# Kernel tuning notes

Measured on AMD Instinct MI355X. Metric: run time of the kernel, lower is better.

## Reference

```python
import jax, jax.numpy as jnp
import numpy as np

LN_EPS = 1e-5


def setup_inputs() -> dict:
    key = jax.random.key(0)
    ks = jax.random.split(key, 4)
    B, N, E, H = 2, 512, 128, 256
    h = jax.random.normal(ks[0], (B, N, E), dtype=jnp.float32)
    gamma = jnp.ones((E,), dtype=jnp.float32)
    beta = jnp.zeros((E,), dtype=jnp.float32)
    # First Linear: in_dim = 2E, out_dim = H. Stored as [2E, H] (x @ W1 + b1).
    W1 = jax.random.normal(ks[1], (2 * E, H), dtype=jnp.float32) / np.sqrt(2 * E)
    b1 = jnp.zeros((H,), dtype=jnp.float32)
    # Second Linear: [H, 1] squeezed to [H], scalar bias.
    w2 = jax.random.normal(ks[2], (H,), dtype=jnp.float32) / np.sqrt(H)
    b2 = jnp.zeros((), dtype=jnp.float32)
    return {"h": h, "gamma": gamma, "beta": beta, "W1": W1, "b1": b1,
            "w2": w2, "b2": b2}


def reference(h, gamma, beta, W1, b1, w2, b2):
    # LayerNorm over E
    mu = jnp.mean(h, axis=-1, keepdims=True)
    var = jnp.mean(jnp.square(h - mu), axis=-1, keepdims=True)
    h_n = (h - mu) * jax.lax.rsqrt(var + LN_EPS) * gamma + beta  # [B,N,E]

    E = h_n.shape[-1]
    # Decompose Linear(concat(h_i, h_j)) = h_i @ Wa + h_j @ Wb + b1
    Wa, Wb = W1[:E], W1[E:]
    a = jnp.einsum('bne,eh->bnh', h_n, Wa)  # contribution of first slot
    b = jnp.einsum('bne,eh->bnh', h_n, Wb)  # contribution of second slot
    # Pairwise pre-activation for the (i,j) ordering: [B,N,N,H]
    z_ij = a[:, :, None, :] + b[:, None, :, :] + b1
    g = jax.nn.gelu(z_ij, approximate=False)  # torch GELU is exact (erf)
    l_ij = jnp.einsum('bijh,h->bij', g, w2) + b2  # [B,N,N]
    # l_ji[b,i,j] == l_ij[b,j,i], so reuse via transpose (same math as
    # running the MLP twice on swapped concat order).
    return 0.5 * (l_ij + jnp.swapaxes(l_ij, 1, 2))
```

## Files before the change

### kernel.cpp

```cpp
#include <hip/hip_runtime.h>
#include <math.h>

#define EDIM 128
#define HDIM 256
#define NDIM 512
#define BDIM 2
#define LN_EPS 1e-5f

typedef float v2f __attribute__((ext_vector_type(2)));

__global__ __launch_bounds__(256) void k_ln_proj(
    const float* __restrict__ hptr, const float* __restrict__ gamma,
    const float* __restrict__ beta, const float* __restrict__ W1,
    const float* __restrict__ b1, float* __restrict__ a_out,
    float* __restrict__ b_out)
{
    __shared__ float hn_s[4][EDIM];
    const int tid = threadIdx.x;
    const int r = tid >> 6;
    const int lane = tid & 63;
    const int row0 = blockIdx.x * 4;
    const float2 v = *(const float2*)(hptr + (row0 + r) * EDIM + lane * 2);
    float s  = v.x + v.y;
    float ss = v.x * v.x + v.y * v.y;
    #pragma unroll
    for (int k = 32; k >= 1; k >>= 1) {
        s  += __shfl_xor(s, k, 64);
        ss += __shfl_xor(ss, k, 64);
    }
    const float mu  = s * (1.0f / EDIM);
    const float var = ss * (1.0f / EDIM) - mu * mu;
    const float rs  = rsqrtf(var + LN_EPS);
    const float2 g2 = *(const float2*)(gamma + lane * 2);
    const float2 be = *(const float2*)(beta + lane * 2);
    hn_s[r][lane * 2]     = (v.x - mu) * rs * g2.x + be.x;
    hn_s[r][lane * 2 + 1] = (v.y - mu) * rs * g2.y + be.y;
    __syncthreads();
    float sa0 = 0.f, sa1 = 0.f, sa2 = 0.f, sa3 = 0.f;
    float sb0 = 0.f, sb1 = 0.f, sb2 = 0.f, sb3 = 0.f;
    #pragma unroll 4
    for (int e = 0; e < EDIM; ++e) {
        const float wa = W1[e * HDIM + tid];
        const float wb = W1[(EDIM + e) * HDIM + tid];
        const float h0 = hn_s[0][e], h1 = hn_s[1][e];
        const float h2 = hn_s[2][e], h3 = hn_s[3][e];
        sa0 = fmaf(h0, wa, sa0); sa1 = fmaf(h1, wa, sa1);
        sa2 = fmaf(h2, wa, sa2); sa3 = fmaf(h3, wa, sa3);
        sb0 = fmaf(h0, wb, sb0); sb1 = fmaf(h1, wb, sb1);
        sb2 = fmaf(h2, wb, sb2); sb3 = fmaf(h3, wb, sb3);
    }
    const float bb1 = b1[tid];
    a_out[(row0 + 0) * HDIM + tid] = sa0;
    a_out[(row0 + 1) * HDIM + tid] = sa1;
    a_out[(row0 + 2) * HDIM + tid] = sa2;
    a_out[(row0 + 3) * HDIM + tid] = sa3;
    b_out[(row0 + 0) * HDIM + tid] = sb0 + bb1;
    b_out[(row0 + 1) * HDIM + tid] = sb1 + bb1;
    b_out[(row0 + 2) * HDIM + tid] = sb2 + bb1;
    b_out[(row0 + 3) * HDIM + tid] = sb3 + bb1;
}

__device__ __forceinline__ v2f gelu2(v2f z) {
    const v2f c2 = {-0.10294826f, -0.10294826f};
    const v2f c1 = {-2.3022082f, -2.3022082f};
    const v2f z2 = z * z;
    const v2f q  = __builtin_elementwise_fma(c2, z2, c1);
    const v2f p  = z * q;
    v2f e;
    e.x = __builtin_amdgcn_exp2f(p.x);
    e.y = __builtin_amdgcn_exp2f(p.y);
    const v2f d = e + 1.0f;
    v2f r;
    r.x = __builtin_amdgcn_rcpf(d.x);
    r.y = __builtin_amdgcn_rcpf(d.y);
    return z * r;
}

#define HHALF 128
#define PAD 132

__global__ __launch_bounds__(256, 6) void k_pair(
    const float* __restrict__ a, const float* __restrict__ bpb,
    const float* __restrict__ w2, float* __restrict__ pout)
{
    __shared__ float a_s[32][PAD];
    __shared__ float b_s[16][PAD];
    __shared__ float w2_s[HHALF];
    const int blk = blockIdx.x;
    const int hh = blk & 1;
    const int bj = (blk >> 1) & 31;
    const int bi = (blk >> 6) & 15;
    const int bb = blk >> 10;
    const int tid = threadIdx.x;
    const int hho = hh * HHALF;

    const float* arow = a + (bb * NDIM + bi * 32) * HDIM + hho;
    const float* brow = bpb + (bb * NDIM + bj * 16) * HDIM + hho;

    if (tid < HHALF / 4) ((float4*)w2_s)[tid] = ((const float4*)(w2 + hho))[tid];

    #pragma unroll
    for (int idx = tid; idx < 1536; idx += 256) {
        if (idx < 1024) {
            const int r = idx >> 5, c = idx & 31;
        *(float4*)&a_s[r][c * 4] = *(const float4*)(arow + r * HDIM + c * 4);
        } else {
            const int k = idx - 1024;
            const int r = k >> 5, c = k & 31;
            *(float4*)&b_s[r][c * 4] = *(const float4*)(brow + r * HDIM + c * 4);
        }
    }
    __syncthreads();

    const int ti = tid >> 4, tj = tid & 15;
    const float* ap0 = a_s[ti];
    const float* ap1 = a_s[ti + 16];
    const float* bp  = b_s[tj];
    v2f acc0 = {0.f, 0.f}, acc1 = {0.f, 0.f};

    #pragma unroll 4
    for (int h4 = 0; h4 < HHALF; h4 += 4) {
        const float4 a0 = *(const float4*)(ap0 + h4);
        const float4 a1 = *(const float4*)(ap1 + h4);
        const float4 b0 = *(const float4*)(bp + h4);
        const float4 wv = *(const float4*)(w2_s + h4);
        const v2f alo0 = {a0.x, a0.y}, ahi0 = {a0.z, a0.w};
        const v2f alo1 = {a1.x, a1.y}, ahi1 = {a1.z, a1.w};
        const v2f blo  = {b0.x, b0.y}, bhi  = {b0.z, b0.w};
        const v2f wlo  = {wv.x, wv.y}, whi  = {wv.z, wv.w};
        acc0 = __builtin_elementwise_fma(wlo, gelu2(alo0 + blo), acc0);
        acc0 = __builtin_elementwise_fma(whi, gelu2(ahi0 + bhi), acc0);
        acc1 = __builtin_elementwise_fma(wlo, gelu2(alo1 + blo), acc1);
        acc1 = __builtin_elementwise_fma(whi, gelu2(ahi1 + bhi), acc1);
    }
    const int i0 = bi * 32 + ti;
    const int j0 = bj * 16 + tj;
    float* ob = pout + (size_t)hh * (BDIM * NDIM * NDIM) + (bb * NDIM + i0) * NDIM + j0;
    ob[0]         = acc0.x + acc0.y;
    ob[16 * NDIM] = acc1.x + acc1.y;
}

__global__ __launch_bounds__(256) void k_sym(const float* __restrict__ p,
                                             float* __restrict__ out,
                                             const float* __restrict__ b2) {
    __shared__ float Ta[32][33];
    __shared__ float Tb[32][33];
    const int blk = blockIdx.x;
    const int b  = blk >> 8;
    const int ti = (blk >> 4) & 15;
    const int tj = blk & 15;
    if (tj < ti) return;
    const float bias = b2[0];
    const float* p0 = p + (size_t)b * NDIM * NDIM;
    const float* p1 = p0 + (size_t)BDIM * NDIM * NDIM;
    float* base = out + (size_t)b * NDIM * NDIM;
    const int tx = threadIdx.x & 31;
    const int ty = threadIdx.x >> 5;
    #pragma unroll
    for (int r = ty; r < 32; r += 8) {
        const int ia = (ti * 32 + r) * NDIM + tj * 32 + tx;
        const int ib = (tj * 32 + r) * NDIM + ti * 32 + tx;
        Ta[r][tx] = p0[ia] + p1[ia];
        Tb[r][tx] = p0[ib] + p1[ib];
    }
    __syncthreads();
    #pragma unroll
    for (int r = ty; r < 32; r += 8) {
        base[(ti * 32 + r) * NDIM + tj * 32 + tx] = 0.5f * (Ta[r][tx] + Tb[tx][r]) + bias;
    }
    if (ti != tj) {
        #pragma unroll
        for (int r = ty; r < 32; r += 8) {
            base[(tj * 32 + r) * NDIM + ti * 32 + tx] = 0.5f * (Tb[r][tx] + Ta[tx][r]) + bias;
        }
    }
}

extern "C" void kernel_launch(void* const* d_in, const int* in_sizes, int n_in,
                              void* d_out, int out_size, void* d_ws, size_t ws_size,
                              hipStream_t stream) {
    const float* hptr  = (const float*)d_in[0];
    const float* gamma = (const float*)d_in[1];
    const float* beta  = (const float*)d_in[2];
    const float* W1    = (const float*)d_in[3];
    const float* b1    = (const float*)d_in[4];
    const float* w2    = (const float*)d_in[5];
    const float* b2    = (const float*)d_in[6];
    float* out = (float*)d_out;

    float* a_ws = (float*)d_ws;
    float* b_ws = a_ws + BDIM * NDIM * HDIM;
    float* p_ws = b_ws + BDIM * NDIM * HDIM;

    k_ln_proj<<<(BDIM * NDIM) / 4, 256, 0, stream>>>(hptr, gamma, beta, W1, b1, a_ws, b_ws);
    k_pair<<<BDIM * 16 * 32 * 2, 256, 0, stream>>>(a_ws, b_ws, w2, p_ws);
    k_sym<<<BDIM * 256, 256, 0, stream>>>(p_ws, out, b2);
}
```

Measured before the change: 48.87 us.

## Replace exp/rcp GELU approximation with shared-memory LUT interpolation

Replaces the sigmoid-based GELU approximation (packed exp2 plus reciprocal) in the pairwise kernel with a 512-entry linear-interpolation table of GELU(|z|)-relu, built in LDS per block using erff. Each element now costs a table lookup, a floor, an fma and a max instead of transcendental instructions, and the packed v2f math becomes scalar. In exchange it adds LDS traffic with possible bank conflicts from the random-index lookups, per-block table construction, and a lower occupancy hint of 5. Accuracy now depends on interpolation step size and clamping at |z|≈16.

Result: slower. 55.53 us (+13.6%).

```diff
diff --git a/kernel.cpp b/kernel.cpp
--- a/kernel.cpp
+++ b/kernel.cpp
@@ -6,8 +6,6 @@
 #define NDIM 512
 #define BDIM 2
 #define LN_EPS 1e-5f
-
-typedef float v2f __attribute__((ext_vector_type(2)));
 
 __global__ __launch_bounds__(256) void k_ln_proj(
     const float* __restrict__ hptr, const float* __restrict__ gamma,
@@ -60,32 +58,22 @@
     b_out[(row0 + 3) * HDIM + tid] = sb3 + bb1;
 }
 
-__device__ __forceinline__ v2f gelu2(v2f z) {
-    const v2f c2 = {-0.10294826f, -0.10294826f};
-    const v2f c1 = {-2.3022082f, -2.3022082f};
-    const v2f z2 = z * z;
-    const v2f q  = __builtin_elementwise_fma(c2, z2, c1);
-    const v2f p  = z * q;
-    v2f e;
-    e.x = __builtin_amdgcn_exp2f(p.x);
-    e.y = __builtin_amdgcn_exp2f(p.y);
-    const v2f d = e + 1.0f;
-    v2f r;
-    r.x = __builtin_amdgcn_rcpf(d.x);
-    r.y = __builtin_amdgcn_rcpf(d.y);
-    return z * r;
-}
+#define LUT_N     512
+#define LUT_H     0.03125f
+#define LUT_SCALE 32.0f
+#define LUT_TMAX  511.49f
 
 #define HHALF 128
 #define PAD 132
 
-__global__ __launch_bounds__(256, 6) void k_pair(
+__global__ __launch_bounds__(256, 5) void k_pair(
     const float* __restrict__ a, const float* __restrict__ bpb,
     const float* __restrict__ w2, float* __restrict__ pout)
 {
     __shared__ float a_s[32][PAD];
     __shared__ float b_s[16][PAD];
     __shared__ float w2_s[HHALF];
+    __shared__ float2 tab[LUT_N];
     const int blk = blockIdx.x;
     const int hh = blk & 1;
     const int bj = (blk >> 1) & 31;
@@ -94,6 +82,15 @@
     const int tid = threadIdx.x;
     const int hho = hh * HHALF;
 
+    #pragma unroll
+    for (int k = tid; k < LUT_N; k += 256) {
+        const float x0 = k * LUT_H;
+        const float x1 = x0 + LUT_H;
+        const float r0 = 0.5f * x0 * (erff(x0 * 0.70710678f) - 1.0f);
+        const float r1 = 0.5f * x1 * (erff(x1 * 0.70710678f) - 1.0f);
+        tab[k] = make_float2(r0, r1 - r0);
+    }
+
     const float* arow = a + (bb * NDIM + bi * 32) * HDIM + hho;
     const float* brow = bpb + (bb * NDIM + bj * 16) * HDIM + hho;
 
@@ -103,7 +100,7 @@
     for (int idx = tid; idx < 1536; idx += 256) {
         if (idx < 1024) {
             const int r = idx >> 5, c = idx & 31;
-        *(float4*)&a_s[r][c * 4] = *(const float4*)(arow + r * HDIM + c * 4);
+            *(float4*)&a_s[r][c * 4] = *(const float4*)(arow + r * HDIM + c * 4);
         } else {
             const int k = idx - 1024;
             const int r = k >> 5, c = k & 31;
@@ -116,7 +113,16 @@
     const float* ap0 = a_s[ti];
     const float* ap1 = a_s[ti + 16];
     const float* bp  = b_s[tj];
-    v2f acc0 = {0.f, 0.f}, acc1 = {0.f, 0.f};
+    float acc0 = 0.f, acc1 = 0.f;
+
+#define GELU_ACC(acc, wv_, av_, bv_) {                         \
+        const float z  = (av_) + (bv_);                        \
+        const float t  = fminf(fabsf(z) * LUT_SCALE, LUT_TMAX);\
+        const float fl = floorf(t);                            \
+        const int   ix = (int)t;                               \
+        const float2 e = tab[ix];                              \
+        const float g  = fmaf(t - fl, e.y, e.x) + fmaxf(z, 0.f);\
+        acc = fmaf((wv_), g, acc); }
 
     #pragma unroll 4
     for (int h4 = 0; h4 < HHALF; h4 += 4) {
@@ -124,20 +130,22 @@
         const float4 a1 = *(const float4*)(ap1 + h4);
         const float4 b0 = *(const float4*)(bp + h4);
         const float4 wv = *(const float4*)(w2_s + h4);
-        const v2f alo0 = {a0.x, a0.y}, ahi0 = {a0.z, a0.w};
-        const v2f alo1 = {a1.x, a1.y}, ahi1 = {a1.z, a1.w};
-        const v2f blo  = {b0.x, b0.y}, bhi  = {b0.z, b0.w};
-        const v2f wlo  = {wv.x, wv.y}, whi  = {wv.z, wv.w};
-        acc0 = __builtin_elementwise_fma(wlo, gelu2(alo0 + blo), acc0);
-        acc0 = __builtin_elementwise_fma(whi, gelu2(ahi0 + bhi), acc0);
-        acc1 = __builtin_elementwise_fma(wlo, gelu2(alo1 + blo), acc1);
-        acc1 = __builtin_elementwise_fma(whi, gelu2(ahi1 + bhi), acc1);
-    }
+        GELU_ACC(acc0, wv.x, a0.x, b0.x);
+        GELU_ACC(acc1, wv.x, a1.x, b0.x);
+        GELU_ACC(acc0, wv.y, a0.y, b0.y);
+        GELU_ACC(acc1, wv.y, a1.y, b0.y);
+        GELU_ACC(acc0, wv.z, a0.z, b0.z);
+        GELU_ACC(acc1, wv.z, a1.z, b0.z);
+        GELU_ACC(acc0, wv.w, a0.w, b0.w);
+        GELU_ACC(acc1, wv.w, a1.w, b0.w);
+    }
+#undef GELU_ACC
+
     const int i0 = bi * 32 + ti;
     const int j0 = bj * 16 + tj;
     float* ob = pout + (size_t)hh * (BDIM * NDIM * NDIM) + (bb * NDIM + i0) * NDIM + j0;
-    ob[0]         = acc0.x + acc0.y;
-    ob[16 * NDIM] = acc1.x + acc1.y;
+    ob[0]         = acc0;
+    ob[16 * NDIM] = acc1;
 }
 
 __global__ __launch_bounds__(256) void k_sym(const float* __restrict__ p,
```

## Split hidden dim into four slices and use scalar GELU in pair kernel

Applied to the files above, without the earlier changes.

The pair kernel now splits the hidden dimension into four 64-wide slices instead of two, doubling the grid and halving shared memory per block. Each slice writes its own partial plane, and the symmetrization kernel sums four planes instead of two. The packed v2f GELU path is replaced with scalar code, and the occupancy hint in launch_bounds is dropped. This raises parallelism and occupancy, at the cost of twice the partial-sum workspace traffic and more redundant tile loads.

After: 57.34 us. 1.17x slower.

```diff
diff --git a/kernel.cpp b/kernel.cpp
--- a/kernel.cpp
+++ b/kernel.cpp
@@ -6,8 +6,6 @@
 #define NDIM 512
 #define BDIM 2
 #define LN_EPS 1e-5f
-
-typedef float v2f __attribute__((ext_vector_type(2)));
 
 __global__ __launch_bounds__(256) void k_ln_proj(
     const float* __restrict__ hptr, const float* __restrict__ gamma,
@@ -60,53 +58,45 @@
     b_out[(row0 + 3) * HDIM + tid] = sb3 + bb1;
 }
 
-__device__ __forceinline__ v2f gelu2(v2f z) {
-    const v2f c2 = {-0.10294826f, -0.10294826f};
-    const v2f c1 = {-2.3022082f, -2.3022082f};
-    const v2f z2 = z * z;
-    const v2f q  = __builtin_elementwise_fma(c2, z2, c1);
-    const v2f p  = z * q;
-    v2f e;
-    e.x = __builtin_amdgcn_exp2f(p.x);
-    e.y = __builtin_amdgcn_exp2f(p.y);
-    const v2f d = e + 1.0f;
-    v2f r;
-    r.x = __builtin_amdgcn_rcpf(d.x);
-    r.y = __builtin_amdgcn_rcpf(d.y);
+__device__ __forceinline__ float gelu_fast(float z) {
+    const float z2 = z * z;
+    const float q  = fmaf(-0.10294826f, z2, -2.3022082f);
+    const float e  = __builtin_amdgcn_exp2f(z * q);
+    const float r  = __builtin_amdgcn_rcpf(1.0f + e);
     return z * r;
 }
 
-#define HHALF 128
-#define PAD 132
+#define HQ 64
+#define PAD 68
 
-__global__ __launch_bounds__(256, 6) void k_pair(
+__global__ __launch_bounds__(256) void k_pair(
     const float* __restrict__ a, const float* __restrict__ bpb,
     const float* __restrict__ w2, float* __restrict__ pout)
 {
     __shared__ float a_s[32][PAD];
     __shared__ float b_s[16][PAD];
-    __shared__ float w2_s[HHALF];
+    __shared__ float w2_s[HQ];
     const int blk = blockIdx.x;
-    const int hh = blk & 1;
-    const int bj = (blk >> 1) & 31;
-    const int bi = (blk >> 6) & 15;
-    const int bb = blk >> 10;
+    const int qq = blk & 3;
+    const int bj = (blk >> 2) & 31;
+    const int bi = (blk >> 7) & 15;
+    const int bb = blk >> 11;
     const int tid = threadIdx.x;
-    const int hho = hh * HHALF;
+    const int hho = qq * HQ;
 
     const float* arow = a + (bb * NDIM + bi * 32) * HDIM + hho;
     const float* brow = bpb + (bb * NDIM + bj * 16) * HDIM + hho;
 
-    if (tid < HHALF / 4) ((float4*)w2_s)[tid] = ((const float4*)(w2 + hho))[tid];
+    if (tid < HQ / 4) ((float4*)w2_s)[tid] = ((const float4*)(w2 + hho))[tid];
 
     #pragma unroll
-    for (int idx = tid; idx < 1536; idx += 256) {
-        if (idx < 1024) {
-            const int r = idx >> 5, c = idx & 31;
-        *(float4*)&a_s[r][c * 4] = *(const float4*)(arow + r * HDIM + c * 4);
+    for (int idx = tid; idx < 768; idx += 256) {
+        if (idx < 512) {
+            const int r = idx >> 4, c = idx & 15;
+            *(float4*)&a_s[r][c * 4] = *(const float4*)(arow + r * HDIM + c * 4);
         } else {
-            const int k = idx - 1024;
-            const int r = k >> 5, c = k & 31;
+            const int k = idx - 512;
+            const int r = k >> 4, c = k & 15;
             *(float4*)&b_s[r][c * 4] = *(const float4*)(brow + r * HDIM + c * 4);
         }
     }
@@ -116,28 +106,29 @@
     const float* ap0 = a_s[ti];
     const float* ap1 = a_s[ti + 16];
     const float* bp  = b_s[tj];
-    v2f acc0 = {0.f, 0.f}, acc1 = {0.f, 0.f};
+    float acc0 = 0.f, acc1 = 0.f;
 
     #pragma unroll 4
-    for (int h4 = 0; h4 < HHALF; h4 += 4) {
+    for (int h4 = 0; h4 < HQ; h4 += 4) {
         const float4 a0 = *(const float4*)(ap0 + h4);
         const float4 a1 = *(const float4*)(ap1 + h4);
         const float4 b0 = *(const float4*)(bp + h4);
         const float4 wv = *(const float4*)(w2_s + h4);
-        const v2f alo0 = {a0.x, a0.y}, ahi0 = {a0.z, a0.w};
-        const v2f alo1 = {a1.x, a1.y}, ahi1 = {a1.z, a1.w};
-        const v2f blo  = {b0.x, b0.y}, bhi  = {b0.z, b0.w};
-        const v2f wlo  = {wv.x, wv.y}, whi  = {wv.z, wv.w};
-        acc0 = __builtin_elementwise_fma(wlo, gelu2(alo0 + blo), acc0);
-        acc0 = __builtin_elementwise_fma(whi, gelu2(ahi0 + bhi), acc0);
-        acc1 = __builtin_elementwise_fma(wlo, gelu2(alo1 + blo), acc1);
-        acc1 = __builtin_elementwise_fma(whi, gelu2(ahi1 + bhi), acc1);
+        acc0 = fmaf(wv.x, gelu_fast(a0.x + b0.x), acc0);
+        acc1 = fmaf(wv.x, gelu_fast(a1.x + b0.x), acc1);
+        acc0 = fmaf(wv.y, gelu_fast(a0.y + b0.y), acc0);
+        acc1 = fmaf(wv.y, gelu_fast(a1.y + b0.y), acc1);
+        acc0 = fmaf(wv.z, gelu_fast(a0.z + b0.z), acc0);
+        acc1 = fmaf(wv.z, gelu_fast(a1.z + b0.z), acc1);
+        acc0 = fmaf(wv.w, gelu_fast(a0.w + b0.w), acc0);
+        acc1 = fmaf(wv.w, gelu_fast(a1.w + b0.w), acc1);
     }
+
     const int i0 = bi * 32 + ti;
     const int j0 = bj * 16 + tj;
-    float* ob = pout + (size_t)hh * (BDIM * NDIM * NDIM) + (bb * NDIM + i0) * NDIM + j0;
-    ob[0]         = acc0.x + acc0.y;
-    ob[16 * NDIM] = acc1.x + acc1.y;
+    float* ob = pout + (size_t)qq * (BDIM * NDIM * NDIM) + (bb * NDIM + i0) * NDIM + j0;
+    ob[0]         = acc0;
+    ob[16 * NDIM] = acc1;
 }
 
 __global__ __launch_bounds__(256) void k_sym(const float* __restrict__ p,
@@ -151,8 +142,8 @@
     const int tj = blk & 15;
     if (tj < ti) return;
     const float bias = b2[0];
+    const size_t plane = (size_t)BDIM * NDIM * NDIM;
     const float* p0 = p + (size_t)b * NDIM * NDIM;
-    const float* p1 = p0 + (size_t)BDIM * NDIM * NDIM;
     float* base = out + (size_t)b * NDIM * NDIM;
     const int tx = threadIdx.x & 31;
     const int ty = threadIdx.x >> 5;
@@ -160,8 +151,8 @@
     for (int r = ty; r < 32; r += 8) {
         const int ia = (ti * 32 + r) * NDIM + tj * 32 + tx;
         const int ib = (tj * 32 + r) * NDIM + ti * 32 + tx;
-        Ta[r][tx] = p0[ia] + p1[ia];
-        Tb[r][tx] = p0[ib] + p1[ib];
+        Ta[r][tx] = (p0[ia] + p0[ia + plane]) + (p0[ia + 2 * plane] + p0[ia + 3 * plane]);
+        Tb[r][tx] = (p0[ib] + p0[ib + plane]) + (p0[ib + 2 * plane] + p0[ib + 3 * plane]);
     }
     __syncthreads();
     #pragma unroll
@@ -193,6 +184,6 @@
     float* p_ws = b_ws + BDIM * NDIM * HDIM;
 
     k_ln_proj<<<(BDIM * NDIM) / 4, 256, 0, stream>>>(hptr, gamma, beta, W1, b1, a_ws, b_ws);
-    k_pair<<<BDIM * 16 * 32 * 2, 256, 0, stream>>>(a_ws, b_ws, w2, p_ws);
+    k_pair<<<BDIM * 16 * 32 * 4, 256, 0, stream>>>(a_ws, b_ws, w2, p_ws);
     k_sym<<<BDIM * 256, 256, 0, stream>>>(p_ws, out, b2);
 }
```
